# Optimization experiments

Measured on AMD Instinct MI355X. Metric: run time of the kernel, lower is better.

Reference implementation:

```python
import jax, jax.numpy as jnp
import numpy as np

DIM = 1024
HEADS = 16
DIM_HEAD = 64
INNER = HEADS * DIM_HEAD  # 1024
SCALE = DIM_HEAD ** -0.5


def setup_inputs() -> dict:
    key = jax.random.key(0)
    k1, k2, k3 = jax.random.split(key, 3)
    x = jax.random.normal(k1, (2, 2048, DIM), dtype=jnp.float32)
    # nn.Linear(dim, inner*3, bias=False): weight [3*inner, dim]; y = x @ W.T
    w_qkv = jax.random.normal(k2, (3 * INNER, DIM), dtype=jnp.float32) * (DIM ** -0.5)
    w_out = jax.random.normal(k3, (DIM, INNER), dtype=jnp.float32) * (INNER ** -0.5)
    return {"x": x, "w_qkv": w_qkv, "w_out": w_out}


def reference(x, w_qkv, w_out):
    b, n, _ = x.shape
    qkv = jnp.einsum('bnd,ed->bne', x, w_qkv)  # [b, n, 3*inner]
    q, k, v = jnp.split(qkv, 3, axis=-1)
    # [b, n, inner] -> [b, heads, n, dim_head]
    def to_heads(t):
        return t.reshape(b, n, HEADS, DIM_HEAD).transpose(0, 2, 1, 3)
    q, k, v = to_heads(q), to_heads(k), to_heads(v)
    dots = jnp.einsum('bhid,bhjd->bhij', q, k) * SCALE  # [b, h, n, n]
    attn = jax.nn.softmax(dots, axis=-1)
    out = jnp.einsum('bhij,bhjd->bhid', attn, v)  # [b, h, n, dim_head]
    out = out.transpose(0, 2, 1, 3).reshape(b, n, INNER)
    return jnp.einsum('bne,de->bnd', out, w_out)
```

## Files before the change

kernel.cpp:

```cpp
#include <hip/hip_runtime.h>
#include <hip/hip_bf16.h>

#define SEQ 2048
#define NTOK 4096
#define DIMK 1024

typedef __attribute__((ext_vector_type(8))) short bf16x8;
typedef __attribute__((ext_vector_type(4))) float f32x4;

__device__ inline short f2bf(float f) {
    __hip_bfloat16 h = __float2bfloat16(f);
    return __builtin_bit_cast(short, h);
}

__device__ inline unsigned pack2bf(float a, float b) {
    unsigned ha = (unsigned short)f2bf(a);
    unsigned hb = (unsigned short)f2bf(b);
    return ha | (hb << 16);
}

__device__ inline void gload16(const void* src, void* lds) {
    __builtin_amdgcn_global_load_lds(
        (const __attribute__((address_space(1))) unsigned int*)src,
        (__attribute__((address_space(3))) unsigned int*)lds, 16, 0, 0);
}

__global__ __launch_bounds__(256) void cast_kernel(const float* __restrict__ in,
                                                   short* __restrict__ out, int n4) {
    int i = blockIdx.x * blockDim.x + threadIdx.x;
    if (i < n4) {
        float4 v = reinterpret_cast<const float4*>(in)[i];
        short4 o;
        o.x = f2bf(v.x); o.y = f2bf(v.y); o.z = f2bf(v.z); o.w = f2bf(v.w);
        reinterpret_cast<short4*>(out)[i] = o;
    }
}

__global__ __launch_bounds__(256) void gemm_qkv(const short* __restrict__ xb,
                                                const short* __restrict__ wb,
                                                short* __restrict__ q,
                                                short* __restrict__ k,
                                                short* __restrict__ vt) {
    __shared__ short Al[128][32];
    __shared__ short Bl[128][32];
    int tid = threadIdx.x;
    int m0 = blockIdx.x * 128;
    int n0 = blockIdx.y * 128;
    int w = tid >> 6, lane = tid & 63, lo = lane & 15, hi = lane >> 4;
    int wm = (w >> 1) * 64, wn = (w & 1) * 64;

    f32x4 acc[4][4];
    for (int a = 0; a < 4; a++)
        for (int b = 0; b < 4; b++)
            for (int r = 0; r < 4; r++) acc[a][b][r] = 0.f;

    int srow = tid >> 2, scol = (tid & 3) * 8;
    int srow1 = (tid + 256) >> 2, scol1 = ((tid + 256) & 3) * 8;

    for (int k0 = 0; k0 < DIMK; k0 += 32) {
        gload16(xb + (size_t)(m0 + srow) * DIMK + k0 + scol, (short*)Al + (w * 64) * 8);
        gload16(xb + (size_t)(m0 + srow1) * DIMK + k0 + scol1, (short*)Al + (256 + w * 64) * 8);
        gload16(wb + (size_t)(n0 + srow) * DIMK + k0 + scol, (short*)Bl + (w * 64) * 8);
        gload16(wb + (size_t)(n0 + srow1) * DIMK + k0 + scol1, (short*)Bl + (256 + w * 64) * 8);
        __syncthreads();
        bf16x8 af[4], bfr[4];
        for (int mt = 0; mt < 4; mt++)
            af[mt] = *reinterpret_cast<const bf16x8*>(&Al[wm + mt * 16 + lo][hi * 8]);
        for (int nt = 0; nt < 4; nt++)
            bfr[nt] = *reinterpret_cast<const bf16x8*>(&Bl[wn + nt * 16 + lo][hi * 8]);
        for (int mt = 0; mt < 4; mt++)
            for (int nt = 0; nt < 4; nt++)
                acc[mt][nt] = __builtin_amdgcn_mfma_f32_16x16x32_bf16(af[mt], bfr[nt],
                                                                      acc[mt][nt], 0, 0, 0);
        __syncthreads();
    }

    for (int mt = 0; mt < 4; mt++) {
        int trow = m0 + wm + mt * 16 + hi * 4;
        for (int nt = 0; nt < 4; nt++) {
            int e = n0 + wn + nt * 16 + lo;
            for (int r = 0; r < 4; r++) {
                float val = acc[mt][nt][r];
                int t = trow + r;
                int b = t >> 11, nn = t & 2047;
                if (e < 1024) {
                    int h = e >> 6, dh = e & 63;
                    q[((size_t)(b * 16 + h) * SEQ + nn) * 64 + dh] = f2bf(val * 0.125f);
                } else if (e < 2048) {
                    int e2 = e - 1024; int h = e2 >> 6, dh = e2 & 63;
                    k[((size_t)(b * 16 + h) * SEQ + nn) * 64 + dh] = f2bf(val);
                } else {
                    int e2 = e - 2048; int h = e2 >> 6, dh = e2 & 63;
                    vt[((size_t)(b * 16 + h) * 64 + dh) * SEQ + nn] = f2bf(val);
                }
            }
        }
    }
}

__global__ __launch_bounds__(256) void attn_kernel(const short* __restrict__ q,
                                                   const short* __restrict__ k,
                                                   const short* __restrict__ vt,
                                                   short* __restrict__ ao) {
    __shared__ short Kl[2][64][64];
    __shared__ short Vl[2][64][64];
    int tid = threadIdx.x;
    int w = tid >> 6, lane = tid & 63, lo = lane & 15, hi = lane >> 4;
    int bh = blockIdx.y;
    int q0 = blockIdx.x * 64 + w * 16;

    const short* qb = q + (size_t)bh * SEQ * 64;
    const short* kb = k + (size_t)bh * SEQ * 64;
    const short* vb = vt + (size_t)bh * 64 * SEQ;

    bf16x8 qf[2];
    for (int j = 0; j < 2; j++)
        qf[j] = *reinterpret_cast<const bf16x8*>(qb + (size_t)(q0 + lo) * 64 + j * 32 + hi * 8);

    int s0row = tid >> 3, s0m = tid & 7;
    int s1row = (tid + 256) >> 3, s1m = (tid + 256) & 7;
    const short* ksrc0 = kb + (size_t)s0row * 64 + ((s0m ^ (s0row & 7)) << 3);
    const short* ksrc1 = kb + (size_t)s1row * 64 + ((s1m ^ (s1row & 7)) << 3);
    const short* vsrc0 = vb + (size_t)s0row * SEQ + ((s0m ^ (s0row & 7)) << 3);
    const short* vsrc1 = vb + (size_t)s1row * SEQ + ((s1m ^ (s1row & 7)) << 3);

    float mrun = -__builtin_inff(), lrun = 0.f;
    f32x4 o[4];
    for (int d = 0; d < 4; d++)
        for (int r = 0; r < 4; r++) o[d][r] = 0.f;

    {
        gload16(ksrc0, (short*)&Kl[0][0][0] + (w * 64) * 8);
        gload16(ksrc1, (short*)&Kl[0][0][0] + (256 + w * 64) * 8);
        gload16(vsrc0, (short*)&Vl[0][0][0] + (w * 64) * 8);
        gload16(vsrc1, (short*)&Vl[0][0][0] + (256 + w * 64) * 8);
    }
    __syncthreads();

    int cur = 0;
    for (int t = 0; t < SEQ / 64; ++t) {
        if (t + 1 < SEQ / 64) {
            int kt = (t + 1) * 64;
            gload16(ksrc0 + kt * 64, (short*)&Kl[cur ^ 1][0][0] + (w * 64) * 8);
            gload16(ksrc1 + kt * 64, (short*)&Kl[cur ^ 1][0][0] + (256 + w * 64) * 8);
            gload16(vsrc0 + kt, (short*)&Vl[cur ^ 1][0][0] + (w * 64) * 8);
            gload16(vsrc1 + kt, (short*)&Vl[cur ^ 1][0][0] + (256 + w * 64) * 8);
        }

        f32x4 s[4];
        #pragma unroll
        for (int sub = 0; sub < 4; ++sub) {
            int row = sub * 16 + lo;
            const short* kp = &Kl[cur][row][0];
            bf16x8 kf0 = *reinterpret_cast<const bf16x8*>(kp + ((hi ^ (row & 7)) << 3));
            bf16x8 kf1 = *reinterpret_cast<const bf16x8*>(kp + (((4 + hi) ^ (row & 7)) << 3));
            f32x4 z = {0.f, 0.f, 0.f, 0.f};
            z = __builtin_amdgcn_mfma_f32_16x16x32_bf16(kf0, qf[0], z, 0, 0, 0);
            z = __builtin_amdgcn_mfma_f32_16x16x32_bf16(kf1, qf[1], z, 0, 0, 0);
            s[sub] = z;
        }

        float pmax = s[0][0];
        #pragma unroll
        for (int sub = 0; sub < 4; ++sub)
            #pragma unroll
            for (int r = 0; r < 4; ++r) pmax = fmaxf(pmax, s[sub][r]);
        pmax = fmaxf(pmax, __shfl_xor(pmax, 16, 64));
        pmax = fmaxf(pmax, __shfl_xor(pmax, 32, 64));
        float mn = fmaxf(mrun, pmax);
        float alpha = __expf(mrun - mn);
        mrun = mn;
        float p[4][4];
        float rs = 0.f;
        #pragma unroll
        for (int sub = 0; sub < 4; ++sub)
            #pragma unroll
            for (int r = 0; r < 4; ++r) {
                float pe = __expf(s[sub][r] - mn);
                p[sub][r] = pe; rs += pe;
            }
        rs += __shfl_xor(rs, 16, 64);
        rs += __shfl_xor(rs, 32, 64);
        lrun = alpha * lrun + rs;
        #pragma unroll
        for (int ds = 0; ds < 4; ++ds)
            #pragma unroll
            for (int r = 0; r < 4; ++r) o[ds][r] *= alpha;

        unsigned pk[4][2];
        #pragma unroll
        for (int sub = 0; sub < 4; ++sub) {
            pk[sub][0] = pack2bf(p[sub][0], p[sub][1]);
            pk[sub][1] = pack2bf(p[sub][2], p[sub][3]);
        }

        #pragma unroll
        for (int koff = 0; koff < 2; ++koff) {
            int pbw[4];
            #pragma unroll
            for (int m = 0; m < 4; ++m) {
                int srcl = ((2 * (hi & 1) + (m >> 1)) << 4) | lo;
                int va = __shfl((int)pk[2 * koff + 0][m & 1], srcl, 64);
                int vb2 = __shfl((int)pk[2 * koff + 1][m & 1], srcl, 64);
                pbw[m] = (hi & 2) ? vb2 : va;
            }
            int4 pbi; pbi.x = pbw[0]; pbi.y = pbw[1]; pbi.z = pbw[2]; pbi.w = pbw[3];
            bf16x8 pb = __builtin_bit_cast(bf16x8, pbi);
            #pragma unroll
            for (int ds = 0; ds < 4; ++ds) {
                int row = ds * 16 + lo;
                bf16x8 vfr = *reinterpret_cast<const bf16x8*>(
                    &Vl[cur][row][0] + (((koff * 4 + hi) ^ (row & 7)) << 3));
                o[ds] = __builtin_amdgcn_mfma_f32_16x16x32_bf16(vfr, pb, o[ds], 0, 0, 0);
            }
        }

        __syncthreads();
        cur ^= 1;
    }

    int b = bh >> 4, h = bh & 15;
    int nn = blockIdx.x * 64 + w * 16 + lo;
    size_t tbase = ((size_t)(b * SEQ + nn)) * 1024 + h * 64;
    float inv = 1.f / lrun;
    #pragma unroll
    for (int ds = 0; ds < 4; ++ds) {
        short4 st;
        st.x = f2bf(o[ds][0] * inv);
        st.y = f2bf(o[ds][1] * inv);
        st.z = f2bf(o[ds][2] * inv);
        st.w = f2bf(o[ds][3] * inv);
        *reinterpret_cast<short4*>(&ao[tbase + ds * 16 + hi * 4]) = st;
    }
}

__global__ __launch_bounds__(256) void gemm_out(const short* __restrict__ a,
                                                const short* __restrict__ b,
                                                float* __restrict__ out) {
    __shared__ short Al[128][32];
    __shared__ short Bl[128][32];
    int tid = threadIdx.x;
    int m0 = blockIdx.x * 128;
    int n0 = blockIdx.y * 128;
    int w = tid >> 6, lane = tid & 63, lo = lane & 15, hi = lane >> 4;
    int wm = (w >> 1) * 64, wn = (w & 1) * 64;

    f32x4 acc[4][4];
    for (int aa = 0; aa < 4; aa++)
        for (int bb = 0; bb < 4; bb++)
            for (int r = 0; r < 4; r++) acc[aa][bb][r] = 0.f;

    int srow = tid >> 2, scol = (tid & 3) * 8;
    int srow1 = (tid + 256) >> 2, scol1 = ((tid + 256) & 3) * 8;

    for (int k0 = 0; k0 < DIMK; k0 += 32) {
        gload16(a + (size_t)(m0 + srow) * DIMK + k0 + scol, (short*)Al + (w * 64) * 8);
        gload16(a + (size_t)(m0 + srow1) * DIMK + k0 + scol1, (short*)Al + (256 + w * 64) * 8);
        gload16(b + (size_t)(n0 + srow) * DIMK + k0 + scol, (short*)Bl + (w * 64) * 8);
        gload16(b + (size_t)(n0 + srow1) * DIMK + k0 + scol1, (short*)Bl + (256 + w * 64) * 8);
        __syncthreads();
        bf16x8 af[4], bfr[4];
        for (int mt = 0; mt < 4; mt++)
            af[mt] = *reinterpret_cast<const bf16x8*>(&Al[wm + mt * 16 + lo][hi * 8]);
        for (int nt = 0; nt < 4; nt++)
            bfr[nt] = *reinterpret_cast<const bf16x8*>(&Bl[wn + nt * 16 + lo][hi * 8]);
        for (int mt = 0; mt < 4; mt++)
            for (int nt = 0; nt < 4; nt++)
                acc[mt][nt] = __builtin_amdgcn_mfma_f32_16x16x32_bf16(af[mt], bfr[nt],
                                                                      acc[mt][nt], 0, 0, 0);
        __syncthreads();
    }

    for (int mt = 0; mt < 4; mt++) {
        int trow = m0 + wm + mt * 16 + hi * 4;
        for (int nt = 0; nt < 4; nt++) {
            int e = n0 + wn + nt * 16 + lo;
            for (int r = 0; r < 4; r++)
                out[(size_t)(trow + r) * 1024 + e] = acc[mt][nt][r];
        }
    }
}

extern "C" void kernel_launch(void* const* d_in, const int* in_sizes, int n_in,
                              void* d_out, int out_size, void* d_ws, size_t ws_size,
                              hipStream_t stream) {
    const float* x = (const float*)d_in[0];
    const float* wqkv = (const float*)d_in[1];
    const float* wout = (const float*)d_in[2];
    float* out = (float*)d_out;

    char* ws = (char*)d_ws;
    short* xb  = (short*)(ws);
    short* wqb = (short*)(ws + 8388608);
    short* wob = (short*)(ws + 8388608 + 6291456);
    short* qq  = (short*)(ws + 16777216);
    short* kk  = (short*)(ws + 25165824);
    short* vt  = (short*)(ws + 33554432);
    short* ao  = xb;

    hipLaunchKernelGGL(cast_kernel, dim3(4096), dim3(256), 0, stream, x, xb, 1048576);
    hipLaunchKernelGGL(cast_kernel, dim3(3072), dim3(256), 0, stream, wqkv, wqb, 786432);
    hipLaunchKernelGGL(cast_kernel, dim3(1024), dim3(256), 0, stream, wqkv ? wout : wout, wob, 262144);
    hipLaunchKernelGGL(gemm_qkv, dim3(32, 24), dim3(256), 0, stream, xb, wqb, qq, kk, vt);
    hipLaunchKernelGGL(attn_kernel, dim3(32, 32), dim3(256), 0, stream, qq, kk, vt, ao);
    hipLaunchKernelGGL(gemm_out, dim3(32, 8), dim3(256), 0, stream, ao, wob, out);
}
```

Before: 159.3 us.

## Widen GEMM K-tile with swizzled LDS and streamline attention softmax

Both GEMMs now stage 64-wide K tiles with an XOR-swizzled LDS layout, halving the number of barrier pairs and avoiding bank conflicts. Attention folds log2(e) into the Q scale so it can use exp2, skips the rescale of the running max when the new max is within a threshold, defers the row-sum reduction to the end, uses packed bf16 conversion, and raises wave priority around the MFMA blocks. These target instruction overhead and synchronisation in the hot loops. The lazy rescale lets probabilities exceed 1 (up to 2^8), which relies on fp32 and bf16 headroom.

Result: slower. 164.6 us (+3.3%).

```diff
diff --git a/kernel.cpp b/kernel.cpp
--- a/kernel.cpp
+++ b/kernel.cpp
@@ -13,10 +13,10 @@
     return __builtin_bit_cast(short, h);
 }
 
-__device__ inline unsigned pack2bf(float a, float b) {
-    unsigned ha = (unsigned short)f2bf(a);
-    unsigned hb = (unsigned short)f2bf(b);
-    return ha | (hb << 16);
+__device__ inline unsigned cvt_pk_bf16(float a, float b) {
+    unsigned r;
+    asm("v_cvt_pk_bf16_f32 %0, %1, %2" : "=v"(r) : "v"(a), "v"(b));
+    return r;
 }
 
 __device__ inline void gload16(const void* src, void* lds) {
@@ -41,8 +41,8 @@
                                                 short* __restrict__ q,
                                                 short* __restrict__ k,
                                                 short* __restrict__ vt) {
-    __shared__ short Al[128][32];
-    __shared__ short Bl[128][32];
+    __shared__ short Al[128][64];
+    __shared__ short Bl[128][64];
     int tid = threadIdx.x;
     int m0 = blockIdx.x * 128;
     int n0 = blockIdx.y * 128;
@@ -54,27 +54,40 @@
         for (int b = 0; b < 4; b++)
             for (int r = 0; r < 4; r++) acc[a][b][r] = 0.f;
 
-    int srow = tid >> 2, scol = (tid & 3) * 8;
-    int srow1 = (tid + 256) >> 2, scol1 = ((tid + 256) & 3) * 8;
-
-    for (int k0 = 0; k0 < DIMK; k0 += 32) {
-        gload16(xb + (size_t)(m0 + srow) * DIMK + k0 + scol, (short*)Al + (w * 64) * 8);
-        gload16(xb + (size_t)(m0 + srow1) * DIMK + k0 + scol1, (short*)Al + (256 + w * 64) * 8);
-        gload16(wb + (size_t)(n0 + srow) * DIMK + k0 + scol, (short*)Bl + (w * 64) * 8);
-        gload16(wb + (size_t)(n0 + srow1) * DIMK + k0 + scol1, (short*)Bl + (256 + w * 64) * 8);
-        __syncthreads();
-        bf16x8 af[4], bfr[4];
-        for (int mt = 0; mt < 4; mt++)
-            af[mt] = *reinterpret_cast<const bf16x8*>(&Al[wm + mt * 16 + lo][hi * 8]);
-        for (int nt = 0; nt < 4; nt++)
-            bfr[nt] = *reinterpret_cast<const bf16x8*>(&Bl[wn + nt * 16 + lo][hi * 8]);
-        for (int mt = 0; mt < 4; mt++)
-            for (int nt = 0; nt < 4; nt++)
-                acc[mt][nt] = __builtin_amdgcn_mfma_f32_16x16x32_bf16(af[mt], bfr[nt],
-                                                                      acc[mt][nt], 0, 0, 0);
-        __syncthreads();
-    }
-
+    for (int k0 = 0; k0 < DIMK; k0 += 64) {
+        #pragma unroll
+        for (int r = 0; r < 4; ++r) {
+            int c = r * 256 + tid;
+            int row = c >> 3, ch = c & 7;
+            int sc = (ch ^ (row & 7)) << 3;
+            gload16(xb + (size_t)(m0 + row) * DIMK + k0 + sc, (short*)Al + (r * 256 + w * 64) * 8);
+            gload16(wb + (size_t)(n0 + row) * DIMK + k0 + sc, (short*)Bl + (r * 256 + w * 64) * 8);
+        }
+        __syncthreads();
+        #pragma unroll
+        for (int j = 0; j < 2; ++j) {
+            bf16x8 af[4], bfr[4];
+            #pragma unroll
+            for (int mt = 0; mt < 4; mt++) {
+                int row = wm + mt * 16 + lo;
+                af[mt] = *reinterpret_cast<const bf16x8*>(&Al[row][((j * 4 + hi) ^ (row & 7)) << 3]);
+            }
+            #pragma unroll
+            for (int nt = 0; nt < 4; nt++) {
+                int row = wn + nt * 16 + lo;
+                bfr[nt] = *reinterpret_cast<const bf16x8*>(&Bl[row][((j * 4 + hi) ^ (row & 7)) << 3]);
+            }
+            #pragma unroll
+            for (int mt = 0; mt < 4; mt++)
+                #pragma unroll
+                for (int nt = 0; nt < 4; nt++)
+                    acc[mt][nt] = __builtin_amdgcn_mfma_f32_16x16x32_bf16(af[mt], bfr[nt],
+                                                                          acc[mt][nt], 0, 0, 0);
+        }
+        __syncthreads();
+    }
+
+    const float QS = 0.125f * 1.44269504088896f;
     for (int mt = 0; mt < 4; mt++) {
         int trow = m0 + wm + mt * 16 + hi * 4;
         for (int nt = 0; nt < 4; nt++) {
@@ -85,7 +98,7 @@
                 int b = t >> 11, nn = t & 2047;
                 if (e < 1024) {
                     int h = e >> 6, dh = e & 63;
-                    q[((size_t)(b * 16 + h) * SEQ + nn) * 64 + dh] = f2bf(val * 0.125f);
+                    q[((size_t)(b * 16 + h) * SEQ + nn) * 64 + dh] = f2bf(val * QS);
                 } else if (e < 2048) {
                     int e2 = e - 1024; int h = e2 >> 6, dh = e2 & 63;
                     k[((size_t)(b * 16 + h) * SEQ + nn) * 64 + dh] = f2bf(val);
@@ -129,12 +142,10 @@
     for (int d = 0; d < 4; d++)
         for (int r = 0; r < 4; r++) o[d][r] = 0.f;
 
-    {
-        gload16(ksrc0, (short*)&Kl[0][0][0] + (w * 64) * 8);
-        gload16(ksrc1, (short*)&Kl[0][0][0] + (256 + w * 64) * 8);
-        gload16(vsrc0, (short*)&Vl[0][0][0] + (w * 64) * 8);
-        gload16(vsrc1, (short*)&Vl[0][0][0] + (256 + w * 64) * 8);
-    }
+    gload16(ksrc0, (short*)&Kl[0][0][0] + (w * 64) * 8);
+    gload16(ksrc1, (short*)&Kl[0][0][0] + (256 + w * 64) * 8);
+    gload16(vsrc0, (short*)&Vl[0][0][0] + (w * 64) * 8);
+    gload16(vsrc1, (short*)&Vl[0][0][0] + (256 + w * 64) * 8);
     __syncthreads();
 
     int cur = 0;
@@ -148,6 +159,7 @@
         }
 
         f32x4 s[4];
+        __builtin_amdgcn_s_setprio(1);
         #pragma unroll
         for (int sub = 0; sub < 4; ++sub) {
             int row = sub * 16 + lo;
@@ -159,6 +171,7 @@
             z = __builtin_amdgcn_mfma_f32_16x16x32_bf16(kf1, qf[1], z, 0, 0, 0);
             s[sub] = z;
         }
+        __builtin_amdgcn_s_setprio(0);
 
         float pmax = s[0][0];
         #pragma unroll
@@ -167,31 +180,33 @@
             for (int r = 0; r < 4; ++r) pmax = fmaxf(pmax, s[sub][r]);
         pmax = fmaxf(pmax, __shfl_xor(pmax, 16, 64));
         pmax = fmaxf(pmax, __shfl_xor(pmax, 32, 64));
-        float mn = fmaxf(mrun, pmax);
-        float alpha = __expf(mrun - mn);
-        mrun = mn;
-        float p[4][4];
+
+        if (!__all(pmax - mrun <= 8.0f)) {
+            float mn = fmaxf(mrun, pmax);
+            float alpha = __builtin_exp2f(mrun - mn);
+            mrun = mn;
+            lrun *= alpha;
+            #pragma unroll
+            for (int ds = 0; ds < 4; ++ds)
+                #pragma unroll
+                for (int r = 0; r < 4; ++r) o[ds][r] *= alpha;
+        }
+
         float rs = 0.f;
         #pragma unroll
         for (int sub = 0; sub < 4; ++sub)
             #pragma unroll
             for (int r = 0; r < 4; ++r) {
-                float pe = __expf(s[sub][r] - mn);
-                p[sub][r] = pe; rs += pe;
-            }
-        rs += __shfl_xor(rs, 16, 64);
-        rs += __shfl_xor(rs, 32, 64);
-        lrun = alpha * lrun + rs;
-        #pragma unroll
-        for (int ds = 0; ds < 4; ++ds)
-            #pragma unroll
-            for (int r = 0; r < 4; ++r) o[ds][r] *= alpha;
+                float pe = __builtin_exp2f(s[sub][r] - mrun);
+                s[sub][r] = pe; rs += pe;
+            }
+        lrun += rs;
 
         unsigned pk[4][2];
         #pragma unroll
         for (int sub = 0; sub < 4; ++sub) {
-            pk[sub][0] = pack2bf(p[sub][0], p[sub][1]);
-            pk[sub][1] = pack2bf(p[sub][2], p[sub][3]);
+            pk[sub][0] = cvt_pk_bf16(s[sub][0], s[sub][1]);
+            pk[sub][1] = cvt_pk_bf16(s[sub][2], s[sub][3]);
         }
 
         #pragma unroll
@@ -206,6 +221,7 @@
             }
             int4 pbi; pbi.x = pbw[0]; pbi.y = pbw[1]; pbi.z = pbw[2]; pbi.w = pbw[3];
             bf16x8 pb = __builtin_bit_cast(bf16x8, pbi);
+            __builtin_amdgcn_s_setprio(1);
             #pragma unroll
             for (int ds = 0; ds < 4; ++ds) {
                 int row = ds * 16 + lo;
@@ -213,32 +229,33 @@
                     &Vl[cur][row][0] + (((koff * 4 + hi) ^ (row & 7)) << 3));
                 o[ds] = __builtin_amdgcn_mfma_f32_16x16x32_bf16(vfr, pb, o[ds], 0, 0, 0);
             }
+            __builtin_amdgcn_s_setprio(0);
         }
 
         __syncthreads();
         cur ^= 1;
     }
 
+    lrun += __shfl_xor(lrun, 16, 64);
+    lrun += __shfl_xor(lrun, 32, 64);
     int b = bh >> 4, h = bh & 15;
     int nn = blockIdx.x * 64 + w * 16 + lo;
     size_t tbase = ((size_t)(b * SEQ + nn)) * 1024 + h * 64;
     float inv = 1.f / lrun;
     #pragma unroll
     for (int ds = 0; ds < 4; ++ds) {
-        short4 st;
-        st.x = f2bf(o[ds][0] * inv);
-        st.y = f2bf(o[ds][1] * inv);
-        st.z = f2bf(o[ds][2] * inv);
-        st.w = f2bf(o[ds][3] * inv);
-        *reinterpret_cast<short4*>(&ao[tbase + ds * 16 + hi * 4]) = st;
+        uint2 st;
+        st.x = cvt_pk_bf16(o[ds][0] * inv, o[ds][1] * inv);
+        st.y = cvt_pk_bf16(o[ds][2] * inv, o[ds][3] * inv);
+        *reinterpret_cast<uint2*>(&ao[tbase + ds * 16 + hi * 4]) = st;
     }
 }
 
 __global__ __launch_bounds__(256) void gemm_out(const short* __restrict__ a,
                                                 const short* __restrict__ b,
                                                 float* __restrict__ out) {
-    __shared__ short Al[128][32];
-    __shared__ short Bl[128][32];
+    __shared__ short Al[128][64];
+    __shared__ short Bl[128][64];
     int tid = threadIdx.x;
     int m0 = blockIdx.x * 128;
     int n0 = blockIdx.y * 128;
@@ -250,24 +267,36 @@
         for (int bb = 0; bb < 4; bb++)
             for (int r = 0; r < 4; r++) acc[aa][bb][r] = 0.f;
 
-    int srow = tid >> 2, scol = (tid & 3) * 8;
-    int srow1 = (tid + 256) >> 2, scol1 = ((tid + 256) & 3) * 8;
-
-    for (int k0 = 0; k0 < DIMK; k0 += 32) {
-        gload16(a + (size_t)(m0 + srow) * DIMK + k0 + scol, (short*)Al + (w * 64) * 8);
-        gload16(a + (size_t)(m0 + srow1) * DIMK + k0 + scol1, (short*)Al + (256 + w * 64) * 8);
-        gload16(b + (size_t)(n0 + srow) * DIMK + k0 + scol, (short*)Bl + (w * 64) * 8);
-        gload16(b + (size_t)(n0 + srow1) * DIMK + k0 + scol1, (short*)Bl + (256 + w * 64) * 8);
-        __syncthreads();
-        bf16x8 af[4], bfr[4];
-        for (int mt = 0; mt < 4; mt++)
-            af[mt] = *reinterpret_cast<const bf16x8*>(&Al[wm + mt * 16 + lo][hi * 8]);
-        for (int nt = 0; nt < 4; nt++)
-            bfr[nt] = *reinterpret_cast<const bf16x8*>(&Bl[wn + nt * 16 + lo][hi * 8]);
-        for (int mt = 0; mt < 4; mt++)
-            for (int nt = 0; nt < 4; nt++)
-                acc[mt][nt] = __builtin_amdgcn_mfma_f32_16x16x32_bf16(af[mt], bfr[nt],
-                                                                      acc[mt][nt], 0, 0, 0);
+    for (int k0 = 0; k0 < DIMK; k0 += 64) {
+        #pragma unroll
+        for (int r = 0; r < 4; ++r) {
+            int c = r * 256 + tid;
+            int row = c >> 3, ch = c & 7;
+            int sc = (ch ^ (row & 7)) << 3;
+            gload16(a + (size_t)(m0 + row) * DIMK + k0 + sc, (short*)Al + (r * 256 + w * 64) * 8);
+            gload16(b + (size_t)(n0 + row) * DIMK + k0 + sc, (short*)Bl + (r * 256 + w * 64) * 8);
+        }
+        __syncthreads();
+        #pragma unroll
+        for (int j = 0; j < 2; ++j) {
+            bf16x8 af[4], bfr[4];
+            #pragma unroll
+            for (int mt = 0; mt < 4; mt++) {
+                int row = wm + mt * 16 + lo;
+                af[mt] = *reinterpret_cast<const bf16x8*>(&Al[row][((j * 4 + hi) ^ (row & 7)) << 3]);
+            }
+            #pragma unroll
+            for (int nt = 0; nt < 4; nt++) {
+                int row = wn + nt * 16 + lo;
+                bfr[nt] = *reinterpret_cast<const bf16x8*>(&Bl[row][((j * 4 + hi) ^ (row & 7)) << 3]);
+            }
+            #pragma unroll
+            for (int mt = 0; mt < 4; mt++)
+                #pragma unroll
+                for (int nt = 0; nt < 4; nt++)
+                    acc[mt][nt] = __builtin_amdgcn_mfma_f32_16x16x32_bf16(af[mt], bfr[nt],
+                                                                          acc[mt][nt], 0, 0, 0);
+        }
         __syncthreads();
     }
 
@@ -300,7 +329,7 @@
 
     hipLaunchKernelGGL(cast_kernel, dim3(4096), dim3(256), 0, stream, x, xb, 1048576);
     hipLaunchKernelGGL(cast_kernel, dim3(3072), dim3(256), 0, stream, wqkv, wqb, 786432);
-    hipLaunchKernelGGL(cast_kernel, dim3(1024), dim3(256), 0, stream, wqkv ? wout : wout, wob, 262144);
+    hipLaunchKernelGGL(cast_kernel, dim3(1024), dim3(256), 0, stream, wout, wob, 262144);
     hipLaunchKernelGGL(gemm_qkv, dim3(32, 24), dim3(256), 0, stream, xb, wqb, qq, kk, vt);
     hipLaunchKernelGGL(attn_kernel, dim3(32, 32), dim3(256), 0, stream, qq, kk, vt, ao);
     hipLaunchKernelGGL(gemm_out, dim3(32, 8), dim3(256), 0, stream, ao, wob, out);
```

## Rewrite attention with 32x32 MFMA tiles, exp2 softmax and lazy rescale; fuse casts

Applied to the files above, without the earlier changes.

The attention kernel is rebuilt around 32x32x16 bf16 MFMA tiles. Each wave now covers 32 query rows, so the grid is halved and every K/V tile loaded into LDS feeds twice as many queries. Softmax uses exp2, with log2(e) folded into the Q scaling in the QKV GEMM epilogue, and skips rescaling the output accumulators unless the running max grows by more than 8. It also adds packed bf16 conversion instructions, s_setprio around the MFMA blocks and a simpler P-fragment exchange using one xor-32 shuffle. The three cast launches are merged into one kernel. The lazy rescale trades some overflow headroom for fewer multiplies, and the larger accumulators raise register pressure.

Result: faster. 149.5 us (-6.2%).

```diff
diff --git a/kernel.cpp b/kernel.cpp
--- a/kernel.cpp
+++ b/kernel.cpp
@@ -2,21 +2,25 @@
 #include <hip/hip_bf16.h>
 
 #define SEQ 2048
-#define NTOK 4096
 #define DIMK 1024
 
 typedef __attribute__((ext_vector_type(8))) short bf16x8;
 typedef __attribute__((ext_vector_type(4))) float f32x4;
+typedef __attribute__((ext_vector_type(16))) float f32x16;
 
 __device__ inline short f2bf(float f) {
     __hip_bfloat16 h = __float2bfloat16(f);
     return __builtin_bit_cast(short, h);
 }
 
-__device__ inline unsigned pack2bf(float a, float b) {
-    unsigned ha = (unsigned short)f2bf(a);
-    unsigned hb = (unsigned short)f2bf(b);
-    return ha | (hb << 16);
+__device__ inline unsigned cvt_pk_bf16(float a, float b) {
+    unsigned r;
+    asm("v_cvt_pk_bf16_f32 %0, %1, %2" : "=v"(r) : "v"(a), "v"(b));
+    return r;
+}
+
+__device__ inline unsigned shx32(unsigned v) {
+    return (unsigned)__shfl_xor((int)v, 32, 64);
 }
 
 __device__ inline void gload16(const void* src, void* lds) {
@@ -25,15 +29,21 @@
         (__attribute__((address_space(3))) unsigned int*)lds, 16, 0, 0);
 }
 
-__global__ __launch_bounds__(256) void cast_kernel(const float* __restrict__ in,
-                                                   short* __restrict__ out, int n4) {
-    int i = blockIdx.x * blockDim.x + threadIdx.x;
-    if (i < n4) {
-        float4 v = reinterpret_cast<const float4*>(in)[i];
-        short4 o;
-        o.x = f2bf(v.x); o.y = f2bf(v.y); o.z = f2bf(v.z); o.w = f2bf(v.w);
-        reinterpret_cast<short4*>(out)[i] = o;
-    }
+__global__ __launch_bounds__(256) void cast3_kernel(const float* __restrict__ x,
+                                                    const float* __restrict__ wqkv,
+                                                    const float* __restrict__ wout,
+                                                    short* __restrict__ xb,
+                                                    short* __restrict__ wqb,
+                                                    short* __restrict__ wob) {
+    int i = blockIdx.x * 256 + threadIdx.x;
+    const float* src; short* dst; int off;
+    if (i < 1048576)      { src = x;    dst = xb;  off = i; }
+    else if (i < 1835008) { src = wqkv; dst = wqb; off = i - 1048576; }
+    else                  { src = wout; dst = wob; off = i - 1835008; }
+    float4 v = reinterpret_cast<const float4*>(src)[off];
+    short4 o;
+    o.x = f2bf(v.x); o.y = f2bf(v.y); o.z = f2bf(v.z); o.w = f2bf(v.w);
+    reinterpret_cast<short4*>(dst)[off] = o;
 }
 
 __global__ __launch_bounds__(256) void gemm_qkv(const short* __restrict__ xb,
@@ -75,6 +85,7 @@
         __syncthreads();
     }
 
+    const float QS = 0.125f * 1.44269504088896f;
     for (int mt = 0; mt < 4; mt++) {
         int trow = m0 + wm + mt * 16 + hi * 4;
         for (int nt = 0; nt < 4; nt++) {
@@ -85,7 +96,7 @@
                 int b = t >> 11, nn = t & 2047;
                 if (e < 1024) {
                     int h = e >> 6, dh = e & 63;
-                    q[((size_t)(b * 16 + h) * SEQ + nn) * 64 + dh] = f2bf(val * 0.125f);
+                    q[((size_t)(b * 16 + h) * SEQ + nn) * 64 + dh] = f2bf(val * QS);
                 } else if (e < 2048) {
                     int e2 = e - 1024; int h = e2 >> 6, dh = e2 & 63;
                     k[((size_t)(b * 16 + h) * SEQ + nn) * 64 + dh] = f2bf(val);
@@ -105,132 +116,145 @@
     __shared__ short Kl[2][64][64];
     __shared__ short Vl[2][64][64];
     int tid = threadIdx.x;
-    int w = tid >> 6, lane = tid & 63, lo = lane & 15, hi = lane >> 4;
+    int w = tid >> 6, lane = tid & 63;
+    int l31 = lane & 31, lh = lane >> 5;
+    bool ishi = (lh != 0);
     int bh = blockIdx.y;
-    int q0 = blockIdx.x * 64 + w * 16;
+    int q0 = blockIdx.x * 128 + w * 32;
 
     const short* qb = q + (size_t)bh * SEQ * 64;
     const short* kb = k + (size_t)bh * SEQ * 64;
     const short* vb = vt + (size_t)bh * 64 * SEQ;
 
-    bf16x8 qf[2];
-    for (int j = 0; j < 2; j++)
-        qf[j] = *reinterpret_cast<const bf16x8*>(qb + (size_t)(q0 + lo) * 64 + j * 32 + hi * 8);
-
-    int s0row = tid >> 3, s0m = tid & 7;
-    int s1row = (tid + 256) >> 3, s1m = (tid + 256) & 7;
-    const short* ksrc0 = kb + (size_t)s0row * 64 + ((s0m ^ (s0row & 7)) << 3);
-    const short* ksrc1 = kb + (size_t)s1row * 64 + ((s1m ^ (s1row & 7)) << 3);
-    const short* vsrc0 = vb + (size_t)s0row * SEQ + ((s0m ^ (s0row & 7)) << 3);
-    const short* vsrc1 = vb + (size_t)s1row * SEQ + ((s1m ^ (s1row & 7)) << 3);
+    bf16x8 qf[4];
+    #pragma unroll
+    for (int ds = 0; ds < 4; ++ds)
+        qf[ds] = *reinterpret_cast<const bf16x8*>(qb + (size_t)(q0 + l31) * 64 + ds * 16 + lh * 8);
+
+    int s0 = tid, s1 = tid + 256;
+    int r0 = s0 >> 3, c0 = s0 & 7;
+    int r1 = s1 >> 3, c1 = s1 & 7;
+    const short* ksrc0 = kb + (size_t)r0 * 64 + ((c0 ^ (r0 & 7)) << 3);
+    const short* ksrc1 = kb + (size_t)r1 * 64 + ((c1 ^ (r1 & 7)) << 3);
+    const short* vsrc0 = vb + (size_t)r0 * SEQ + ((c0 ^ (r0 & 7)) << 3);
+    const short* vsrc1 = vb + (size_t)r1 * SEQ + ((c1 ^ (r1 & 7)) << 3);
 
     float mrun = -__builtin_inff(), lrun = 0.f;
-    f32x4 o[4];
-    for (int d = 0; d < 4; d++)
-        for (int r = 0; r < 4; r++) o[d][r] = 0.f;
-
-    {
-        gload16(ksrc0, (short*)&Kl[0][0][0] + (w * 64) * 8);
-        gload16(ksrc1, (short*)&Kl[0][0][0] + (256 + w * 64) * 8);
-        gload16(vsrc0, (short*)&Vl[0][0][0] + (w * 64) * 8);
-        gload16(vsrc1, (short*)&Vl[0][0][0] + (256 + w * 64) * 8);
-    }
+    f32x16 o0, o1;
+    #pragma unroll
+    for (int i = 0; i < 16; ++i) { o0[i] = 0.f; o1[i] = 0.f; }
+
+    gload16(ksrc0, (short*)&Kl[0][0][0] + (w * 64) * 8);
+    gload16(ksrc1, (short*)&Kl[0][0][0] + (256 + w * 64) * 8);
+    gload16(vsrc0, (short*)&Vl[0][0][0] + (w * 64) * 8);
+    gload16(vsrc1, (short*)&Vl[0][0][0] + (256 + w * 64) * 8);
     __syncthreads();
 
     int cur = 0;
     for (int t = 0; t < SEQ / 64; ++t) {
         if (t + 1 < SEQ / 64) {
             int kt = (t + 1) * 64;
-            gload16(ksrc0 + kt * 64, (short*)&Kl[cur ^ 1][0][0] + (w * 64) * 8);
-            gload16(ksrc1 + kt * 64, (short*)&Kl[cur ^ 1][0][0] + (256 + w * 64) * 8);
+            gload16(ksrc0 + (size_t)kt * 64, (short*)&Kl[cur ^ 1][0][0] + (w * 64) * 8);
+            gload16(ksrc1 + (size_t)kt * 64, (short*)&Kl[cur ^ 1][0][0] + (256 + w * 64) * 8);
             gload16(vsrc0 + kt, (short*)&Vl[cur ^ 1][0][0] + (w * 64) * 8);
             gload16(vsrc1 + kt, (short*)&Vl[cur ^ 1][0][0] + (256 + w * 64) * 8);
         }
 
-        f32x4 s[4];
         #pragma unroll
-        for (int sub = 0; sub < 4; ++sub) {
-            int row = sub * 16 + lo;
-            const short* kp = &Kl[cur][row][0];
-            bf16x8 kf0 = *reinterpret_cast<const bf16x8*>(kp + ((hi ^ (row & 7)) << 3));
-            bf16x8 kf1 = *reinterpret_cast<const bf16x8*>(kp + (((4 + hi) ^ (row & 7)) << 3));
-            f32x4 z = {0.f, 0.f, 0.f, 0.f};
-            z = __builtin_amdgcn_mfma_f32_16x16x32_bf16(kf0, qf[0], z, 0, 0, 0);
-            z = __builtin_amdgcn_mfma_f32_16x16x32_bf16(kf1, qf[1], z, 0, 0, 0);
-            s[sub] = z;
-        }
-
-        float pmax = s[0][0];
-        #pragma unroll
-        for (int sub = 0; sub < 4; ++sub)
+        for (int kt32 = 0; kt32 < 2; ++kt32) {
+            int krow = kt32 * 32 + l31;
+            const short* kp = &Kl[cur][krow][0];
+            f32x16 s;
             #pragma unroll
-            for (int r = 0; r < 4; ++r) pmax = fmaxf(pmax, s[sub][r]);
-        pmax = fmaxf(pmax, __shfl_xor(pmax, 16, 64));
-        pmax = fmaxf(pmax, __shfl_xor(pmax, 32, 64));
-        float mn = fmaxf(mrun, pmax);
-        float alpha = __expf(mrun - mn);
-        mrun = mn;
-        float p[4][4];
-        float rs = 0.f;
-        #pragma unroll
-        for (int sub = 0; sub < 4; ++sub)
-            #pragma unroll
-            for (int r = 0; r < 4; ++r) {
-                float pe = __expf(s[sub][r] - mn);
-                p[sub][r] = pe; rs += pe;
-            }
-        rs += __shfl_xor(rs, 16, 64);
-        rs += __shfl_xor(rs, 32, 64);
-        lrun = alpha * lrun + rs;
-        #pragma unroll
-        for (int ds = 0; ds < 4; ++ds)
-            #pragma unroll
-            for (int r = 0; r < 4; ++r) o[ds][r] *= alpha;
-
-        unsigned pk[4][2];
-        #pragma unroll
-        for (int sub = 0; sub < 4; ++sub) {
-            pk[sub][0] = pack2bf(p[sub][0], p[sub][1]);
-            pk[sub][1] = pack2bf(p[sub][2], p[sub][3]);
-        }
-
-        #pragma unroll
-        for (int koff = 0; koff < 2; ++koff) {
-            int pbw[4];
-            #pragma unroll
-            for (int m = 0; m < 4; ++m) {
-                int srcl = ((2 * (hi & 1) + (m >> 1)) << 4) | lo;
-                int va = __shfl((int)pk[2 * koff + 0][m & 1], srcl, 64);
-                int vb2 = __shfl((int)pk[2 * koff + 1][m & 1], srcl, 64);
-                pbw[m] = (hi & 2) ? vb2 : va;
-            }
-            int4 pbi; pbi.x = pbw[0]; pbi.y = pbw[1]; pbi.z = pbw[2]; pbi.w = pbw[3];
-            bf16x8 pb = __builtin_bit_cast(bf16x8, pbi);
+            for (int i = 0; i < 16; ++i) s[i] = 0.f;
+            __builtin_amdgcn_s_setprio(1);
             #pragma unroll
             for (int ds = 0; ds < 4; ++ds) {
-                int row = ds * 16 + lo;
-                bf16x8 vfr = *reinterpret_cast<const bf16x8*>(
-                    &Vl[cur][row][0] + (((koff * 4 + hi) ^ (row & 7)) << 3));
-                o[ds] = __builtin_amdgcn_mfma_f32_16x16x32_bf16(vfr, pb, o[ds], 0, 0, 0);
-            }
+                bf16x8 kf = *reinterpret_cast<const bf16x8*>(
+                    kp + (((ds * 2 + lh) ^ (krow & 7)) << 3));
+                s = __builtin_amdgcn_mfma_f32_32x32x16_bf16(kf, qf[ds], s, 0, 0, 0);
+            }
+            __builtin_amdgcn_s_setprio(0);
+
+            float pmax = s[0];
+            #pragma unroll
+            for (int i = 1; i < 16; ++i) pmax = fmaxf(pmax, s[i]);
+            pmax = fmaxf(pmax, __shfl_xor(pmax, 32, 64));
+            if (!__all(pmax - mrun <= 8.0f)) {
+                float mn = fmaxf(mrun, pmax);
+                float al = __builtin_exp2f(mrun - mn);
+                mrun = mn; lrun *= al;
+                #pragma unroll
+                for (int i = 0; i < 16; ++i) { o0[i] *= al; o1[i] *= al; }
+            }
+            float rs = 0.f;
+            #pragma unroll
+            for (int i = 0; i < 16; ++i) {
+                float p = __builtin_exp2f(s[i] - mrun);
+                s[i] = p; rs += p;
+            }
+            rs += __shfl_xor(rs, 32, 64);
+            lrun += rs;
+
+            unsigned A0 = cvt_pk_bf16(s[0], s[1]),   A1 = cvt_pk_bf16(s[2], s[3]);
+            unsigned B0 = cvt_pk_bf16(s[4], s[5]),   B1 = cvt_pk_bf16(s[6], s[7]);
+            unsigned C0 = cvt_pk_bf16(s[8], s[9]),   C1 = cvt_pk_bf16(s[10], s[11]);
+            unsigned D0 = cvt_pk_bf16(s[12], s[13]), D1 = cvt_pk_bf16(s[14], s[15]);
+            unsigned E0 = ishi ? A0 : B0;
+            unsigned E1 = ishi ? A1 : B1;
+            unsigned F0 = ishi ? C0 : D0;
+            unsigned F1 = ishi ? C1 : D1;
+            unsigned pE0 = shx32(E0), pE1 = shx32(E1);
+            unsigned pF0 = shx32(F0), pF1 = shx32(F1);
+            int4 f0i, f1i;
+            f0i.x = (int)(ishi ? pE0 : A0);
+            f0i.y = (int)(ishi ? pE1 : A1);
+            f0i.z = (int)(ishi ? B0 : pE0);
+            f0i.w = (int)(ishi ? B1 : pE1);
+            f1i.x = (int)(ishi ? pF0 : C0);
+            f1i.y = (int)(ishi ? pF1 : C1);
+            f1i.z = (int)(ishi ? D0 : pF0);
+            f1i.w = (int)(ishi ? D1 : pF1);
+            bf16x8 pf0 = __builtin_bit_cast(bf16x8, f0i);
+            bf16x8 pf1 = __builtin_bit_cast(bf16x8, f1i);
+
+            int vrow0 = l31, vrow1 = 32 + l31;
+            const short* vp0 = &Vl[cur][vrow0][0];
+            const short* vp1 = &Vl[cur][vrow1][0];
+            __builtin_amdgcn_s_setprio(1);
+            {
+                int kg = kt32 * 2;
+                bf16x8 v00 = *reinterpret_cast<const bf16x8*>(vp0 + (((kg * 2 + lh) ^ (vrow0 & 7)) << 3));
+                o0 = __builtin_amdgcn_mfma_f32_32x32x16_bf16(v00, pf0, o0, 0, 0, 0);
+                bf16x8 v10 = *reinterpret_cast<const bf16x8*>(vp1 + (((kg * 2 + lh) ^ (vrow1 & 7)) << 3));
+                o1 = __builtin_amdgcn_mfma_f32_32x32x16_bf16(v10, pf0, o1, 0, 0, 0);
+                kg = kt32 * 2 + 1;
+                bf16x8 v01 = *reinterpret_cast<const bf16x8*>(vp0 + (((kg * 2 + lh) ^ (vrow0 & 7)) << 3));
+                o0 = __builtin_amdgcn_mfma_f32_32x32x16_bf16(v01, pf1, o0, 0, 0, 0);
+                bf16x8 v11 = *reinterpret_cast<const bf16x8*>(vp1 + (((kg * 2 + lh) ^ (vrow1 & 7)) << 3));
+                o1 = __builtin_amdgcn_mfma_f32_32x32x16_bf16(v11, pf1, o1, 0, 0, 0);
+            }
+            __builtin_amdgcn_s_setprio(0);
         }
 
         __syncthreads();
         cur ^= 1;
     }
 
+    float inv = 1.f / lrun;
     int b = bh >> 4, h = bh & 15;
-    int nn = blockIdx.x * 64 + w * 16 + lo;
-    size_t tbase = ((size_t)(b * SEQ + nn)) * 1024 + h * 64;
-    float inv = 1.f / lrun;
+    int qrow = q0 + l31;
+    short* aop = ao + ((size_t)(b * SEQ + qrow)) * 1024 + h * 64;
     #pragma unroll
-    for (int ds = 0; ds < 4; ++ds) {
-        short4 st;
-        st.x = f2bf(o[ds][0] * inv);
-        st.y = f2bf(o[ds][1] * inv);
-        st.z = f2bf(o[ds][2] * inv);
-        st.w = f2bf(o[ds][3] * inv);
-        *reinterpret_cast<short4*>(&ao[tbase + ds * 16 + hi * 4]) = st;
+    for (int g = 0; g < 4; ++g) {
+        uint2 u;
+        u.x = cvt_pk_bf16(o0[4 * g] * inv, o0[4 * g + 1] * inv);
+        u.y = cvt_pk_bf16(o0[4 * g + 2] * inv, o0[4 * g + 3] * inv);
+        *reinterpret_cast<uint2*>(aop + 8 * g + 4 * lh) = u;
+        uint2 v;
+        v.x = cvt_pk_bf16(o1[4 * g] * inv, o1[4 * g + 1] * inv);
+        v.y = cvt_pk_bf16(o1[4 * g + 2] * inv, o1[4 * g + 3] * inv);
+        *reinterpret_cast<uint2*>(aop + 32 + 8 * g + 4 * lh) = v;
     }
 }
 
@@ -298,10 +322,8 @@
     short* vt  = (short*)(ws + 33554432);
     short* ao  = xb;
 
-    hipLaunchKernelGGL(cast_kernel, dim3(4096), dim3(256), 0, stream, x, xb, 1048576);
-    hipLaunchKernelGGL(cast_kernel, dim3(3072), dim3(256), 0, stream, wqkv, wqb, 786432);
-    hipLaunchKernelGGL(cast_kernel, dim3(1024), dim3(256), 0, stream, wqkv ? wout : wout, wob, 262144);
+    hipLaunchKernelGGL(cast3_kernel, dim3(8192), dim3(256), 0, stream, x, wqkv, wout, xb, wqb, wob);
     hipLaunchKernelGGL(gemm_qkv, dim3(32, 24), dim3(256), 0, stream, xb, wqb, qq, kk, vt);
-    hipLaunchKernelGGL(attn_kernel, dim3(32, 32), dim3(256), 0, stream, qq, kk, vt, ao);
+    hipLaunchKernelGGL(attn_kernel, dim3(16, 32), dim3(256), 0, stream, qq, kk, vt, ao);
     hipLaunchKernelGGL(gemm_out, dim3(32, 8), dim3(256), 0, stream, ao, wob, out);
 }
```
